# Kernel optimization log

Measured on AMD Instinct MI355X. Metric: run time of the kernel, lower is better.

The kernel has to match this reference:

```python
import jax, jax.numpy as jnp
import numpy as np

N, D = 16384, 16     # nodes (hits), node feature dim (= embedding dim, slice is full)
K = 64               # max_num_neighbors
MAX_RADIUS = 6.0     # kNN radius cut
PID_MAX = 5000


def setup_inputs() -> dict:
    key = jax.random.key(0)
    k1, k2 = jax.random.split(key)
    x = jax.random.normal(k1, (N, D), dtype=jnp.float32)
    particle_id = jax.random.randint(k2, (N,), 0, PID_MAX, dtype=jnp.int32)
    return {"x": x, "particle_id": particle_id}


def reference(x, particle_id):
    # ml is None and embedding_slice=(None,None) -> embedding features are x itself
    emb = x
    # knn_graph: squared pairwise distances, self-loops excluded (diag = +inf)
    sq = jnp.sum(emb * emb, axis=1)                       # [N]
    d2 = sq[:, None] + sq[None, :] - 2.0 * (emb @ emb.T)  # [N, N]
    diag = jnp.arange(N)
    d2 = d2.at[diag, diag].set(jnp.inf)
    _, nbr = jax.lax.top_k(-d2, K)                        # [N, K] nearest neighbor ids
    src = nbr.reshape(-1)                                 # edge_index[0]: neighbor (source)
    dst = jnp.repeat(jnp.arange(N, dtype=src.dtype), K)   # edge_index[1]: query node
    # radius filter: keep edges with dist < max_radius (fixed shape -> boolean mask)
    diff = x[src] - x[dst]                                # [N*K, D]
    dists = jnp.sqrt(jnp.maximum(jnp.sum(diff * diff, axis=1), 0.0))
    mask = dists < MAX_RADIUS                             # [N*K]
    # edge truth labels: same (nonzero) particle id on both ends
    y = (particle_id[src] == particle_id[dst]) & (particle_id[src] > 0) & mask
    # edge features: [x_src - x_dst, x_src + x_dst], zeroed on masked-out edges
    edge_features = jnp.concatenate([diff, x[src] + x[dst]], axis=1)
    edge_features = edge_features * mask[:, None].astype(x.dtype)
    edge_index = jnp.stack([src, dst])                    # [2, N*K]
    return x, edge_index, y.astype(jnp.int32), edge_features, mask
```

## Files before the change

### kernel.cpp

```cpp
#include <hip/hip_runtime.h>

#define NN 16384
#define DD 16
#define KK 64
#define QQ 4
#define TPB 256
#define HIST 1024
#define HISTW (HIST/2)
#define LIST_MAX 1024
#define CAND_MAX 256

__device__ __forceinline__ float halving_sumsq16(const float* v) {
    float p[16];
#pragma unroll
    for (int d = 0; d < 16; ++d) p[d] = __fmul_rn(v[d], v[d]);
    float r8[8];
#pragma unroll
    for (int j = 0; j < 8; ++j) r8[j] = __fadd_rn(p[j], p[j + 8]);
    float r4[4];
#pragma unroll
    for (int j = 0; j < 4; ++j) r4[j] = __fadd_rn(r8[j], r8[j + 4]);
    float r2[2];
#pragma unroll
    for (int j = 0; j < 2; ++j) r2[j] = __fadd_rn(r4[j], r4[j + 2]);
    return __fadd_rn(r2[0], r2[1]);
}

__device__ __forceinline__ float d2_of(const float* xi, const float* xj,
                                       float sqi, float sqj) {
    float dot = 0.0f;
#pragma unroll
    for (int d = 0; d < DD; ++d) dot = fmaf(xi[d], xj[d], dot);
    return __fsub_rn(__fadd_rn(sqi, sqj), __fmul_rn(2.0f, dot));
}

__device__ __forceinline__ int bucket_of(float d2) {
    int b = (int)__fmul_rn(d2, 4.0f);
    if (b < 0) b = 0;
    if (b >= HIST) b = HIST - 1;
    return b;
}

__global__ void prep_kernel(const float* __restrict__ x,
                            float* __restrict__ out_x,
                            float* __restrict__ sqf) {
    int i = blockIdx.x * blockDim.x + threadIdx.x;
    if (i < NN) {
        float v[DD];
#pragma unroll
        for (int d = 0; d < DD; ++d) v[d] = x[i * DD + d];
        sqf[i] = halving_sumsq16(v);
    }
    for (int t = i; t < NN * DD; t += gridDim.x * blockDim.x) {
        out_x[t] = x[t];
    }
}

__global__ __launch_bounds__(TPB) void knn_kernel(
        const float* __restrict__ x,
        const int* __restrict__ pid,
        const float* __restrict__ sqf,
        float* __restrict__ out_src,
        float* __restrict__ out_dst,
        float* __restrict__ out_y,
        float* __restrict__ out_ef,
        float* __restrict__ out_mask) {
    __shared__ unsigned int hist[QQ][HISTW];
    __shared__ unsigned short list[QQ][LIST_MAX];
    __shared__ unsigned int cand_key[QQ][CAND_MAX];
    __shared__ int cand_idx[QQ][CAND_MAX];
    __shared__ unsigned int wavesum[QQ][TPB / 64];
    __shared__ int s_bsel[QQ];
    __shared__ unsigned int s_listcnt[QQ], s_candcnt[QQ];
    __shared__ int s_fb[QQ];

    const int bid = blockIdx.x;
    const int tid = threadIdx.x;
    const int lane = tid & 63;
    const int w = tid >> 6;
    const int iA = bid * QQ;

    for (int t = tid; t < QQ * HISTW; t += TPB)
        ((unsigned int*)hist)[t] = 0;
    if (tid < QQ) { s_listcnt[tid] = 0; s_candcnt[tid] = 0; s_bsel[tid] = HIST - 1; }

    float xq[QQ][DD];
    float sq[QQ], Tq[QQ];
#pragma unroll
    for (int q = 0; q < QQ; ++q) {
        const float4* p = reinterpret_cast<const float4*>(x + (iA + q) * DD);
        float4 a0 = p[0], a1 = p[1], a2 = p[2], a3 = p[3];
        xq[q][0]=a0.x; xq[q][1]=a0.y; xq[q][2]=a0.z; xq[q][3]=a0.w;
        xq[q][4]=a1.x; xq[q][5]=a1.y; xq[q][6]=a1.z; xq[q][7]=a1.w;
        xq[q][8]=a2.x; xq[q][9]=a2.y; xq[q][10]=a2.z; xq[q][11]=a2.w;
        xq[q][12]=a3.x; xq[q][13]=a3.y; xq[q][14]=a3.z; xq[q][15]=a3.w;
        sq[q] = sqf[iA + q];
        Tq[q] = 16.0f + sq[q] - 1.8f * sqrtf(32.0f + 4.0f * sq[q]);
    }
    __syncthreads();

    for (int j = tid; j < NN; j += TPB) {
        const float4* xj4 = reinterpret_cast<const float4*>(x + j * DD);
        float4 a0 = xj4[0], a1 = xj4[1], a2 = xj4[2], a3 = xj4[3];
        float xj[DD] = {a0.x, a0.y, a0.z, a0.w, a1.x, a1.y, a1.z, a1.w,
                        a2.x, a2.y, a2.z, a2.w, a3.x, a3.y, a3.z, a3.w};
        const float sj = sqf[j];
#pragma unroll
        for (int q = 0; q < QQ; ++q) {
            float d2 = d2_of(xq[q], xj, sq[q], sj);
            bool want = d2 < Tq[q];
            unsigned long long m = __ballot(want);
            if (want) {
                int leader = __ffsll(m) - 1;
                unsigned int base = 0;
                if (lane == leader)
                    base = atomicAdd(&s_listcnt[q], (unsigned int)__popcll(m));
                base = __shfl(base, leader, 64);
                unsigned int pos =
                    base + (unsigned int)__popcll(m & ((1ull << lane) - 1ull));
                if (pos < LIST_MAX) list[q][pos] = (unsigned short)j;
            }
        }
    }
    __syncthreads();

    if (tid < QQ)
        s_fb[tid] = (s_listcnt[tid] < KK + 1) || (s_listcnt[tid] > LIST_MAX);
    __syncthreads();
    const int anyfb = s_fb[0] | s_fb[1] | s_fb[2] | s_fb[3];

    if (anyfb) {
        for (int j = tid; j < NN; j += TPB) {
            const float4* xj4 = reinterpret_cast<const float4*>(x + j * DD);
            float4 a0 = xj4[0], a1 = xj4[1], a2 = xj4[2], a3 = xj4[3];
            float xj[DD] = {a0.x, a0.y, a0.z, a0.w, a1.x, a1.y, a1.z, a1.w,
                            a2.x, a2.y, a2.z, a2.w, a3.x, a3.y, a3.z, a3.w};
            const float sj = sqf[j];
#pragma unroll
            for (int q = 0; q < QQ; ++q) {
                if (s_fb[q] && j != iA + q) {
                    float d2 = d2_of(xq[q], xj, sq[q], sj);
                    int b = bucket_of(d2);
                    atomicAdd(&hist[q][b >> 1], 1u << ((b & 1) << 4));
                }
            }
        }
    }

#pragma unroll
    for (int q = 0; q < QQ; ++q) {
        if (!s_fb[q]) {
            const int lc = (int)s_listcnt[q];
            for (int e = tid; e < lc; e += TPB) {
                const int j = list[q][e];
                const float4* xj4 = reinterpret_cast<const float4*>(x + j * DD);
                float4 a0 = xj4[0], a1 = xj4[1], a2 = xj4[2], a3 = xj4[3];
                float xj[DD] = {a0.x, a0.y, a0.z, a0.w, a1.x, a1.y, a1.z, a1.w,
                                a2.x, a2.y, a2.z, a2.w, a3.x, a3.y, a3.z, a3.w};
                float d2 = d2_of(xq[q], xj, sq[q], sqf[j]);
                int b = bucket_of(d2);
                atomicAdd(&hist[q][b >> 1], 1u << ((b & 1) << 4));
            }
        }
    }
    __syncthreads();

    {
        unsigned int local[QQ], inc[QQ];
        unsigned int pc0[QQ], pc1[QQ], pc2[QQ], pc3[QQ];
#pragma unroll
        for (int q = 0; q < QQ; ++q) {
            unsigned int h0 = hist[q][2 * tid];
            unsigned int h1 = hist[q][2 * tid + 1];
            pc0[q] = h0 & 0xFFFFu; pc1[q] = h0 >> 16;
            pc2[q] = h1 & 0xFFFFu; pc3[q] = h1 >> 16;
            unsigned int s = pc0[q] + pc1[q] + pc2[q] + pc3[q];
            local[q] = s;
            unsigned int v = s;
#pragma unroll
            for (int off = 1; off < 64; off <<= 1) {
                unsigned int n = __shfl_up(v, off, 64);
                if (lane >= off) v += n;
            }
            inc[q] = v;
        }
        if (lane == 63)
#pragma unroll
            for (int q = 0; q < QQ; ++q) wavesum[q][w] = inc[q];
        __syncthreads();
#pragma unroll
        for (int q = 0; q < QQ; ++q) {
            const unsigned int need = s_fb[q] ? KK : (KK + 1);
            unsigned int woff = 0;
            for (int ww = 0; ww < w; ++ww) woff += wavesum[q][ww];
            unsigned int cum = inc[q] + woff;
            unsigned int prev = cum - local[q];
            if (prev < need && need <= cum) {
                unsigned int acc = prev;
                int b = 4 * tid;
                if (acc + pc0[q] < need) { acc += pc0[q]; ++b;
                    if (acc + pc1[q] < need) { acc += pc1[q]; ++b;
                        if (acc + pc2[q] < need) { acc += pc2[q]; ++b; } } }
                s_bsel[q] = b;
            }
        }
    }
    __syncthreads();

#pragma unroll
    for (int q = 0; q < QQ; ++q) {
        if (!s_fb[q]) {
            const int bsel = s_bsel[q];
            const int lc = (int)s_listcnt[q];
            for (int e = tid; e < lc; e += TPB) {
                const int j = list[q][e];
                const float4* xj4 = reinterpret_cast<const float4*>(x + j * DD);
                float4 a0 = xj4[0], a1 = xj4[1], a2 = xj4[2], a3 = xj4[3];
                float xj[DD] = {a0.x, a0.y, a0.z, a0.w, a1.x, a1.y, a1.z, a1.w,
                                a2.x, a2.y, a2.z, a2.w, a3.x, a3.y, a3.z, a3.w};
                float d2 = d2_of(xq[q], xj, sq[q], sqf[j]);
                if (bucket_of(d2) <= bsel && j != iA + q) {
                    unsigned int pos = atomicAdd(&s_candcnt[q], 1u);
                    if (pos < CAND_MAX) {
                        unsigned int u = __float_as_uint(d2);
                        u ^= (u & 0x80000000u) ? 0xFFFFFFFFu : 0x80000000u;
                        cand_key[q][pos] = u;
                        cand_idx[q][pos] = j;
                    }
                }
            }
        }
    }
    if (anyfb) {
        for (int j = tid; j < NN; j += TPB) {
            const float4* xj4 = reinterpret_cast<const float4*>(x + j * DD);
            float4 a0 = xj4[0], a1 = xj4[1], a2 = xj4[2], a3 = xj4[3];
            float xj[DD] = {a0.x, a0.y, a0.z, a0.w, a1.x, a1.y, a1.z, a1.w,
                            a2.x, a2.y, a2.z, a2.w, a3.x, a3.y, a3.z, a3.w};
            const float sj = sqf[j];
#pragma unroll
            for (int q = 0; q < QQ; ++q) {
                if (s_fb[q] && j != iA + q) {
                    float d2 = d2_of(xq[q], xj, sq[q], sj);
                    if (bucket_of(d2) <= s_bsel[q]) {
                        unsigned int pos = atomicAdd(&s_candcnt[q], 1u);
                        if (pos < CAND_MAX) {
                            unsigned int u = __float_as_uint(d2);
                            u ^= (u & 0x80000000u) ? 0xFFFFFFFFu : 0x80000000u;
                            cand_key[q][pos] = u;
                            cand_idx[q][pos] = j;
                        }
                    }
                }
            }
        }
    }
    __syncthreads();

    for (int q = 0; q < QQ; ++q) {
        const int iq = iA + q;
        const int mypid = pid[iq];
        int c = (int)s_candcnt[q];
        if (c > CAND_MAX) c = CAND_MAX;
        for (int t = tid; t < c; t += TPB) {
            const unsigned int kt = cand_key[q][t];
            const int jt = cand_idx[q][t];
            int rank = 0;
            for (int u = 0; u < c; ++u) {
                unsigned int ku = cand_key[q][u];
                rank += (ku < kt) || (ku == kt && cand_idx[q][u] < jt);
            }
            if (rank < KK) {
                const long e = (long)iq * KK + rank;
                out_src[e] = (float)jt;

                const float* xj = x + jt * DD;
                float diff[DD], sum[DD];
#pragma unroll
                for (int d = 0; d < DD; ++d) {
                    float a = xj[d], b = xq[q][d];
                    diff[d] = __fsub_rn(a, b);
                    sum[d]  = __fadd_rn(a, b);
                }
                const float s2 = halving_sumsq16(diff);
                const bool m = __fsqrt_rn(s2) < 6.0f;
                out_mask[e] = m ? 1.0f : 0.0f;
                const int pj = pid[jt];
                out_y[e] = (m && pj == mypid && pj > 0) ? 1.0f : 0.0f;

                float* ef = out_ef + e * (2 * DD);
#pragma unroll
                for (int d = 0; d < DD; ++d) ef[d] = m ? diff[d] : 0.0f;
#pragma unroll
                for (int d = 0; d < DD; ++d) ef[DD + d] = m ? sum[d] : 0.0f;
            }
        }
    }

    for (int t = tid; t < QQ * KK; t += TPB) {
        out_dst[(long)iA * KK + t] = (float)(iA + t / KK);
    }
}

extern "C" void kernel_launch(void* const* d_in, const int* in_sizes, int n_in,
                              void* d_out, int out_size, void* d_ws, size_t ws_size,
                              hipStream_t stream) {
    const float* x = (const float*)d_in[0];
    const int* pid = (const int*)d_in[1];
    float* out = (float*)d_out;

    float* out_x   = out;
    float* out_src = out_x + NN * DD;
    float* out_dst = out_src + NN * KK;
    float* out_y   = out_dst + NN * KK;
    float* out_ef  = out_y + NN * KK;
    float* out_mask = out_ef + (long)NN * KK * 2 * DD;

    float* sqf = (float*)d_ws;

    prep_kernel<<<NN / 256, 256, 0, stream>>>(x, out_x, sqf);
    knn_kernel<<<NN / QQ, TPB, 0, stream>>>(x, pid, sqf, out_src, out_dst,
                                            out_y, out_ef, out_mask);
}
```

Before: 394.4 us.

## Replace per-candidate ballot+atomic list append with bitmask and prefix-scan compaction

The first distance pass no longer does a ballot, shared atomic and shuffle for each query and each point. It records threshold hits as per-thread bitmasks in shared memory, then builds the candidate lists with popcounts, a wave prefix scan and a cross-wave sum, writing each index to a precomputed slot. This removes divergent atomic and shuffle traffic from the hot loop. In exchange it adds 8 KB of shared memory, which may lower occupancy, and changes list ordering to be deterministic.

```diff
diff --git a/kernel.cpp b/kernel.cpp
--- a/kernel.cpp
+++ b/kernel.cpp
@@ -5,6 +5,7 @@
 #define KK 64
 #define QQ 4
 #define TPB 256
+#define NCHUNK 8
 #define HIST 1024
 #define HISTW (HIST/2)
 #define LIST_MAX 1024
@@ -65,10 +66,12 @@
         float* __restrict__ out_y,
         float* __restrict__ out_ef,
         float* __restrict__ out_mask) {
+    __shared__ unsigned int bm[NCHUNK][TPB];
     __shared__ unsigned int hist[QQ][HISTW];
     __shared__ unsigned short list[QQ][LIST_MAX];
     __shared__ unsigned int cand_key[QQ][CAND_MAX];
     __shared__ int cand_idx[QQ][CAND_MAX];
+    __shared__ unsigned int wcnt[TPB / 64][QQ];
     __shared__ unsigned int wavesum[QQ][TPB / 64];
     __shared__ int s_bsel[QQ];
     __shared__ unsigned int s_listcnt[QQ], s_candcnt[QQ];
@@ -82,7 +85,7 @@
 
     for (int t = tid; t < QQ * HISTW; t += TPB)
         ((unsigned int*)hist)[t] = 0;
-    if (tid < QQ) { s_listcnt[tid] = 0; s_candcnt[tid] = 0; s_bsel[tid] = HIST - 1; }
+    if (tid < QQ) { s_candcnt[tid] = 0; s_bsel[tid] = HIST - 1; }
 
     float xq[QQ][DD];
     float sq[QQ], Tq[QQ];
@@ -99,26 +102,69 @@
     }
     __syncthreads();
 
-    for (int j = tid; j < NN; j += TPB) {
-        const float4* xj4 = reinterpret_cast<const float4*>(x + j * DD);
-        float4 a0 = xj4[0], a1 = xj4[1], a2 = xj4[2], a3 = xj4[3];
-        float xj[DD] = {a0.x, a0.y, a0.z, a0.w, a1.x, a1.y, a1.z, a1.w,
-                        a2.x, a2.y, a2.z, a2.w, a3.x, a3.y, a3.z, a3.w};
-        const float sj = sqf[j];
+    for (int c = 0; c < NCHUNK; ++c) {
+        unsigned int bits = 0;
+#pragma unroll
+        for (int k = 0; k < 8; ++k) {
+            const int j = (c * 8 + k) * TPB + tid;
+            const float4* xj4 = reinterpret_cast<const float4*>(x + j * DD);
+            float4 a0 = xj4[0], a1 = xj4[1], a2 = xj4[2], a3 = xj4[3];
+            float xj[DD] = {a0.x, a0.y, a0.z, a0.w, a1.x, a1.y, a1.z, a1.w,
+                            a2.x, a2.y, a2.z, a2.w, a3.x, a3.y, a3.z, a3.w};
+            const float sj = sqf[j];
+#pragma unroll
+            for (int q = 0; q < QQ; ++q) {
+                float d2 = d2_of(xq[q], xj, sq[q], sj);
+                if (d2 < Tq[q]) bits |= (1u << (4 * k + q));
+            }
+        }
+        bm[c][tid] = bits;
+    }
+    __syncthreads();
+
+    {
+        unsigned int cnt[QQ] = {0, 0, 0, 0};
+        for (int c = 0; c < NCHUNK; ++c) {
+            unsigned int w32 = bm[c][tid];
+#pragma unroll
+            for (int q = 0; q < QQ; ++q)
+                cnt[q] += (unsigned int)__popc(w32 & (0x11111111u << q));
+        }
+        unsigned int incl[QQ], excl[QQ];
 #pragma unroll
         for (int q = 0; q < QQ; ++q) {
-            float d2 = d2_of(xq[q], xj, sq[q], sj);
-            bool want = d2 < Tq[q];
-            unsigned long long m = __ballot(want);
-            if (want) {
-                int leader = __ffsll(m) - 1;
-                unsigned int base = 0;
-                if (lane == leader)
-                    base = atomicAdd(&s_listcnt[q], (unsigned int)__popcll(m));
-                base = __shfl(base, leader, 64);
-                unsigned int pos =
-                    base + (unsigned int)__popcll(m & ((1ull << lane) - 1ull));
-                if (pos < LIST_MAX) list[q][pos] = (unsigned short)j;
+            unsigned int v = cnt[q];
+#pragma unroll
+            for (int off = 1; off < 64; off <<= 1) {
+                unsigned int n = __shfl_up(v, off, 64);
+                if (lane >= off) v += n;
+            }
+            incl[q] = v;
+            excl[q] = v - cnt[q];
+        }
+        if (lane == 63)
+#pragma unroll
+            for (int q = 0; q < QQ; ++q) wcnt[w][q] = incl[q];
+        __syncthreads();
+        if (tid < QQ)
+            s_listcnt[tid] = wcnt[0][tid] + wcnt[1][tid] + wcnt[2][tid] + wcnt[3][tid];
+        unsigned int cur[QQ];
+#pragma unroll
+        for (int q = 0; q < QQ; ++q) {
+            unsigned int b = 0;
+            for (int ww = 0; ww < w; ++ww) b += wcnt[ww][q];
+            cur[q] = b + excl[q];
+        }
+        for (int c = 0; c < NCHUNK; ++c) {
+            unsigned int w32 = bm[c][tid];
+            while (w32) {
+                int b = __ffs(w32) - 1;
+                int q = b & 3;
+                int k = b >> 2;
+                unsigned int pos = cur[q]++;
+                if (pos < LIST_MAX)
+                    list[q][pos] = (unsigned short)((c * 8 + k) * TPB + tid);
+                w32 &= w32 - 1;
             }
         }
     }
```

Result: slower. 416.6 us (+5.6%).

## Split kNN kernel into scan and select kernels via workspace candidate lists

Applied to the files above, without the earlier changes.

Splits the monolithic kNN kernel into a lean scan kernel that only filters candidates into a per-query list, and a select kernel that reloads the list from workspace and does the histogram, candidate selection and output. The goal is to shrink the shared memory and register footprint of the heavy brute-force scan so more blocks fit per CU. It also lowers LIST_MAX and recomputes the in-threshold count in the select kernel to decide fallback. The cost is an extra launch and a global round trip for the lists, plus the added risk of more fallback cases now that list overflow happens at a smaller size.

```diff
diff --git a/kernel.cpp b/kernel.cpp
--- a/kernel.cpp
+++ b/kernel.cpp
@@ -7,7 +7,7 @@
 #define TPB 256
 #define HIST 1024
 #define HISTW (HIST/2)
-#define LIST_MAX 1024
+#define LIST_MAX 768
 #define CAND_MAX 256
 
 __device__ __forceinline__ float halving_sumsq16(const float* v) {
@@ -40,6 +40,26 @@
     if (b >= HIST) b = HIST - 1;
     return b;
 }
+
+#define LOAD_XQ()                                                              \
+    float xq[QQ][DD];                                                          \
+    float sq[QQ], Tq[QQ];                                                      \
+    _Pragma("unroll") for (int q = 0; q < QQ; ++q) {                           \
+        const float4* p = reinterpret_cast<const float4*>(x + (iA + q) * DD);  \
+        float4 a0 = p[0], a1 = p[1], a2 = p[2], a3 = p[3];                     \
+        xq[q][0]=a0.x; xq[q][1]=a0.y; xq[q][2]=a0.z; xq[q][3]=a0.w;            \
+        xq[q][4]=a1.x; xq[q][5]=a1.y; xq[q][6]=a1.z; xq[q][7]=a1.w;            \
+        xq[q][8]=a2.x; xq[q][9]=a2.y; xq[q][10]=a2.z; xq[q][11]=a2.w;          \
+        xq[q][12]=a3.x; xq[q][13]=a3.y; xq[q][14]=a3.z; xq[q][15]=a3.w;        \
+        sq[q] = sqf[iA + q];                                                   \
+        Tq[q] = 16.0f + sq[q] - 1.8f * sqrtf(32.0f + 4.0f * sq[q]);            \
+    }
+
+#define LOAD_XJ(j)                                                             \
+    const float4* xj4 = reinterpret_cast<const float4*>(x + (j) * DD);         \
+    float4 a0 = xj4[0], a1 = xj4[1], a2 = xj4[2], a3 = xj4[3];                 \
+    float xj[DD] = {a0.x, a0.y, a0.z, a0.w, a1.x, a1.y, a1.z, a1.w,            \
+                    a2.x, a2.y, a2.z, a2.w, a3.x, a3.y, a3.z, a3.w};
 
 __global__ void prep_kernel(const float* __restrict__ x,
                             float* __restrict__ out_x,
@@ -56,54 +76,25 @@
     }
 }
 
-__global__ __launch_bounds__(TPB) void knn_kernel(
+__global__ __launch_bounds__(TPB) void scan_kernel(
         const float* __restrict__ x,
-        const int* __restrict__ pid,
         const float* __restrict__ sqf,
-        float* __restrict__ out_src,
-        float* __restrict__ out_dst,
-        float* __restrict__ out_y,
-        float* __restrict__ out_ef,
-        float* __restrict__ out_mask) {
-    __shared__ unsigned int hist[QQ][HISTW];
+        unsigned int* __restrict__ ws_cnt,
+        unsigned short* __restrict__ ws_list) {
     __shared__ unsigned short list[QQ][LIST_MAX];
-    __shared__ unsigned int cand_key[QQ][CAND_MAX];
-    __shared__ int cand_idx[QQ][CAND_MAX];
-    __shared__ unsigned int wavesum[QQ][TPB / 64];
-    __shared__ int s_bsel[QQ];
-    __shared__ unsigned int s_listcnt[QQ], s_candcnt[QQ];
-    __shared__ int s_fb[QQ];
+    __shared__ unsigned int s_cnt[QQ];
 
     const int bid = blockIdx.x;
     const int tid = threadIdx.x;
     const int lane = tid & 63;
-    const int w = tid >> 6;
     const int iA = bid * QQ;
 
-    for (int t = tid; t < QQ * HISTW; t += TPB)
-        ((unsigned int*)hist)[t] = 0;
-    if (tid < QQ) { s_listcnt[tid] = 0; s_candcnt[tid] = 0; s_bsel[tid] = HIST - 1; }
-
-    float xq[QQ][DD];
-    float sq[QQ], Tq[QQ];
-#pragma unroll
-    for (int q = 0; q < QQ; ++q) {
-        const float4* p = reinterpret_cast<const float4*>(x + (iA + q) * DD);
-        float4 a0 = p[0], a1 = p[1], a2 = p[2], a3 = p[3];
-        xq[q][0]=a0.x; xq[q][1]=a0.y; xq[q][2]=a0.z; xq[q][3]=a0.w;
-        xq[q][4]=a1.x; xq[q][5]=a1.y; xq[q][6]=a1.z; xq[q][7]=a1.w;
-        xq[q][8]=a2.x; xq[q][9]=a2.y; xq[q][10]=a2.z; xq[q][11]=a2.w;
-        xq[q][12]=a3.x; xq[q][13]=a3.y; xq[q][14]=a3.z; xq[q][15]=a3.w;
-        sq[q] = sqf[iA + q];
-        Tq[q] = 16.0f + sq[q] - 1.8f * sqrtf(32.0f + 4.0f * sq[q]);
-    }
+    if (tid < QQ) s_cnt[tid] = 0;
+    LOAD_XQ();
     __syncthreads();
 
     for (int j = tid; j < NN; j += TPB) {
-        const float4* xj4 = reinterpret_cast<const float4*>(x + j * DD);
-        float4 a0 = xj4[0], a1 = xj4[1], a2 = xj4[2], a3 = xj4[3];
-        float xj[DD] = {a0.x, a0.y, a0.z, a0.w, a1.x, a1.y, a1.z, a1.w,
-                        a2.x, a2.y, a2.z, a2.w, a3.x, a3.y, a3.z, a3.w};
+        LOAD_XJ(j);
         const float sj = sqf[j];
 #pragma unroll
         for (int q = 0; q < QQ; ++q) {
@@ -114,7 +105,7 @@
                 int leader = __ffsll(m) - 1;
                 unsigned int base = 0;
                 if (lane == leader)
-                    base = atomicAdd(&s_listcnt[q], (unsigned int)__popcll(m));
+                    base = atomicAdd(&s_cnt[q], (unsigned int)__popcll(m));
                 base = __shfl(base, leader, 64);
                 unsigned int pos =
                     base + (unsigned int)__popcll(m & ((1ull << lane) - 1ull));
@@ -124,17 +115,87 @@
     }
     __syncthreads();
 
+    for (int q = 0; q < QQ; ++q) {
+        int lc = (int)min(s_cnt[q], (unsigned int)LIST_MAX);
+        unsigned short* dst = ws_list + ((long)iA + q) * LIST_MAX;
+        for (int e = tid; e < lc; e += TPB) dst[e] = list[q][e];
+    }
+    if (tid < QQ) ws_cnt[iA + tid] = s_cnt[tid];
+}
+
+__global__ __launch_bounds__(TPB) void select_kernel(
+        const float* __restrict__ x,
+        const int* __restrict__ pid,
+        const float* __restrict__ sqf,
+        const unsigned int* __restrict__ ws_cnt,
+        const unsigned short* __restrict__ ws_list,
+        float* __restrict__ out_src,
+        float* __restrict__ out_dst,
+        float* __restrict__ out_y,
+        float* __restrict__ out_ef,
+        float* __restrict__ out_mask) {
+    __shared__ unsigned short list[QQ][LIST_MAX];
+    __shared__ unsigned int hist[QQ][HISTW];
+    __shared__ unsigned int cand_key[QQ][CAND_MAX];
+    __shared__ int cand_idx[QQ][CAND_MAX];
+    __shared__ unsigned int wavesum[QQ][TPB / 64];
+    __shared__ int s_bsel[QQ];
+    __shared__ unsigned int s_excnt[QQ], s_candcnt[QQ], s_lc[QQ];
+    __shared__ int s_fb[QQ];
+
+    const int bid = blockIdx.x;
+    const int tid = threadIdx.x;
+    const int lane = tid & 63;
+    const int w = tid >> 6;
+    const int iA = bid * QQ;
+
+    for (int t = tid; t < QQ * HISTW; t += TPB)
+        ((unsigned int*)hist)[t] = 0;
+    if (tid < QQ) {
+        s_excnt[tid] = 0; s_candcnt[tid] = 0; s_bsel[tid] = HIST - 1;
+        s_lc[tid] = min(ws_cnt[iA + tid], (unsigned int)LIST_MAX);
+    }
+    LOAD_XQ();
+    __syncthreads();
+
+    for (int q = 0; q < QQ; ++q) {
+        const unsigned short* src = ws_list + ((long)iA + q) * LIST_MAX;
+        const int lc = (int)s_lc[q];
+        for (int e = tid; e < lc; e += TPB) list[q][e] = src[e];
+    }
+    __syncthreads();
+
+    for (int q = 0; q < QQ; ++q) {
+        const int lc = (int)s_lc[q];
+        unsigned int my = 0;
+        for (int e = tid; e < lc; e += TPB) {
+            const int j = list[q][e];
+            LOAD_XJ(j);
+            float d2 = d2_of(xq[q], xj, sq[q], sqf[j]);
+            my += (d2 < Tq[q]) ? 1u : 0u;
+            int b = bucket_of(d2);
+            atomicAdd(&hist[q][b >> 1], 1u << ((b & 1) << 4));
+        }
+        unsigned int v = my;
+#pragma unroll
+        for (int off = 1; off < 64; off <<= 1) v += __shfl_xor(v, off, 64);
+        if (lane == 0 && v) atomicAdd(&s_excnt[q], v);
+    }
+    __syncthreads();
+
     if (tid < QQ)
-        s_fb[tid] = (s_listcnt[tid] < KK + 1) || (s_listcnt[tid] > LIST_MAX);
+        s_fb[tid] = (ws_cnt[iA + tid] > LIST_MAX) || (s_excnt[tid] < KK + 1);
     __syncthreads();
     const int anyfb = s_fb[0] | s_fb[1] | s_fb[2] | s_fb[3];
 
     if (anyfb) {
+#pragma unroll
+        for (int q = 0; q < QQ; ++q)
+            if (s_fb[q])
+                for (int t = tid; t < HISTW; t += TPB) hist[q][t] = 0;
+        __syncthreads();
         for (int j = tid; j < NN; j += TPB) {
-            const float4* xj4 = reinterpret_cast<const float4*>(x + j * DD);
-            float4 a0 = xj4[0], a1 = xj4[1], a2 = xj4[2], a3 = xj4[3];
-            float xj[DD] = {a0.x, a0.y, a0.z, a0.w, a1.x, a1.y, a1.z, a1.w,
-                            a2.x, a2.y, a2.z, a2.w, a3.x, a3.y, a3.z, a3.w};
+            LOAD_XJ(j);
             const float sj = sqf[j];
 #pragma unroll
             for (int q = 0; q < QQ; ++q) {
@@ -143,23 +204,6 @@
                     int b = bucket_of(d2);
                     atomicAdd(&hist[q][b >> 1], 1u << ((b & 1) << 4));
                 }
-            }
-        }
-    }
-
-#pragma unroll
-    for (int q = 0; q < QQ; ++q) {
-        if (!s_fb[q]) {
-            const int lc = (int)s_listcnt[q];
-            for (int e = tid; e < lc; e += TPB) {
-                const int j = list[q][e];
-                const float4* xj4 = reinterpret_cast<const float4*>(x + j * DD);
-                float4 a0 = xj4[0], a1 = xj4[1], a2 = xj4[2], a3 = xj4[3];
-                float xj[DD] = {a0.x, a0.y, a0.z, a0.w, a1.x, a1.y, a1.z, a1.w,
-                                a2.x, a2.y, a2.z, a2.w, a3.x, a3.y, a3.z, a3.w};
-                float d2 = d2_of(xq[q], xj, sq[q], sqf[j]);
-                int b = bucket_of(d2);
-                atomicAdd(&hist[q][b >> 1], 1u << ((b & 1) << 4));
             }
         }
     }
@@ -211,13 +255,10 @@
     for (int q = 0; q < QQ; ++q) {
         if (!s_fb[q]) {
             const int bsel = s_bsel[q];
-            const int lc = (int)s_listcnt[q];
+            const int lc = (int)s_lc[q];
             for (int e = tid; e < lc; e += TPB) {
                 const int j = list[q][e];
-                const float4* xj4 = reinterpret_cast<const float4*>(x + j * DD);
-                float4 a0 = xj4[0], a1 = xj4[1], a2 = xj4[2], a3 = xj4[3];
-                float xj[DD] = {a0.x, a0.y, a0.z, a0.w, a1.x, a1.y, a1.z, a1.w,
-                                a2.x, a2.y, a2.z, a2.w, a3.x, a3.y, a3.z, a3.w};
+                LOAD_XJ(j);
                 float d2 = d2_of(xq[q], xj, sq[q], sqf[j]);
                 if (bucket_of(d2) <= bsel && j != iA + q) {
                     unsigned int pos = atomicAdd(&s_candcnt[q], 1u);
@@ -233,10 +274,7 @@
     }
     if (anyfb) {
         for (int j = tid; j < NN; j += TPB) {
-            const float4* xj4 = reinterpret_cast<const float4*>(x + j * DD);
-            float4 a0 = xj4[0], a1 = xj4[1], a2 = xj4[2], a3 = xj4[3];
-            float xj[DD] = {a0.x, a0.y, a0.z, a0.w, a1.x, a1.y, a1.z, a1.w,
-                            a2.x, a2.y, a2.z, a2.w, a3.x, a3.y, a3.z, a3.w};
+            LOAD_XJ(j);
             const float sj = sqf[j];
 #pragma unroll
             for (int q = 0; q < QQ; ++q) {
@@ -274,11 +312,11 @@
                 const long e = (long)iq * KK + rank;
                 out_src[e] = (float)jt;
 
-                const float* xj = x + jt * DD;
+                const float* xjp = x + jt * DD;
                 float diff[DD], sum[DD];
 #pragma unroll
                 for (int d = 0; d < DD; ++d) {
-                    float a = xj[d], b = xq[q][d];
+                    float a = xjp[d], b = xq[q][d];
                     diff[d] = __fsub_rn(a, b);
                     sum[d]  = __fadd_rn(a, b);
                 }
@@ -317,8 +355,13 @@
     float* out_mask = out_ef + (long)NN * KK * 2 * DD;
 
     float* sqf = (float*)d_ws;
+    unsigned int* ws_cnt = (unsigned int*)((char*)d_ws + NN * sizeof(float));
+    unsigned short* ws_list =
+        (unsigned short*)((char*)d_ws + NN * sizeof(float) + NN * sizeof(unsigned int));
 
     prep_kernel<<<NN / 256, 256, 0, stream>>>(x, out_x, sqf);
-    knn_kernel<<<NN / QQ, TPB, 0, stream>>>(x, pid, sqf, out_src, out_dst,
-                                            out_y, out_ef, out_mask);
-}
+    scan_kernel<<<NN / QQ, TPB, 0, stream>>>(x, sqf, ws_cnt, ws_list);
+    select_kernel<<<NN / QQ, TPB, 0, stream>>>(x, pid, sqf, ws_cnt, ws_list,
+                                               out_src, out_dst, out_y,
+                                               out_ef, out_mask);
+}
```

After: 426.5 us. +8.2%, slower.
